# Performance work log

Measured on AMD Instinct MI355X. Metric: run time of the kernel, lower is better.

The kernel has to match this reference:

```python
import jax, jax.numpy as jnp
import numpy as np

H = 128            # hidden_channels
HM = 2 * H         # _inner_mlp_mult * H
N = 50000          # num nodes
E = 400000         # num edges
M = 800000         # num node-edge incidences (2 per edge)
BN_EPS = 1e-5


def _bn_relu(x, g, b):
    # BatchNorm1d in training mode: population stats over the batch dim, then affine + ReLU
    m = x.mean(0)
    v = ((x - m) ** 2).mean(0)
    return jax.nn.relu((x - m) * jax.lax.rsqrt(v + BN_EPS) * g + b)


def setup_inputs() -> dict:
    key = jax.random.key(0)
    ks = jax.random.split(key, 12)
    node_rep = jax.random.normal(ks[0], (N, H), dtype=jnp.float32)
    edge_rep = jax.random.normal(ks[1], (E, H), dtype=jnp.float32)
    src = jax.random.randint(ks[2], (M,), 0, N, dtype=jnp.int32)
    dst = jax.random.randint(ks[3], (M,), 0, E, dtype=jnp.int32)
    node2edge_index = jnp.stack([src, dst], 0)

    def lin(k, fan_in, fan_out):
        return jax.random.normal(k, (fan_in, fan_out), dtype=jnp.float32) / np.sqrt(fan_in)

    return {
        "node_rep": node_rep,
        "edge_rep": edge_rep,
        "node2edge_index": node2edge_index,
        # lvl_mlp_1: Linear(2H->H, no bias), BN(H), ReLU
        "Wa": lin(ks[4], 2 * H, H), "ga": jnp.ones((H,)), "ba": jnp.zeros((H,)),
        # lvl_mlp_2: Linear(H->2H), BN, ReLU, Linear(2H->H), BN, ReLU
        "Wb1": lin(ks[5], H, HM), "gb1": jnp.ones((HM,)), "bb1": jnp.zeros((HM,)),
        "Wb2": lin(ks[6], HM, H), "gb2": jnp.ones((H,)), "bb2": jnp.zeros((H,)),
        # lift_mlp: Linear(H->2H), BN, ReLU, Linear(2H->H), BN, ReLU
        "Wl1": lin(ks[7], H, HM), "gl1": jnp.ones((HM,)), "bl1": jnp.zeros((HM,)),
        "Wl2": lin(ks[8], HM, H), "gl2": jnp.ones((H,)), "bl2": jnp.zeros((H,)),
        "eps1": jnp.zeros(()), "eps2": jnp.zeros(()),
    }


def reference(node_rep, edge_rep, node2edge_index,
              Wa, ga, ba,
              Wb1, gb1, bb1, Wb2, gb2, bb2,
              Wl1, gl1, bl1, Wl2, gl2, bl2,
              eps1, eps2):
    src = node2edge_index[0]  # node index per incidence
    dst = node2edge_index[1]  # edge index per incidence

    # node -> edge gather + scatter_sum
    node2edge_val = node_rep[src]                                   # [M, H]
    lift_aggr = jax.ops.segment_sum(node2edge_val, dst, num_segments=E)  # [E, H]

    # lvl_mlp_1 on concatenated edge features
    lvl_aggr_edge = _bn_relu(jnp.concatenate([lift_aggr, edge_rep], -1) @ Wa, ga, ba)  # [E, H]

    # edge -> node gather + scatter_sum
    lvl_aggr = jax.ops.segment_sum(lvl_aggr_edge[dst], src, num_segments=N)  # [N, H]

    # lvl_mlp_2
    hn = (1.0 + eps1) * node_rep + lvl_aggr
    node_out = _bn_relu(_bn_relu(hn @ Wb1, gb1, bb1) @ Wb2, gb2, bb2)

    # lift_mlp
    he = (1.0 + eps2) * edge_rep + lift_aggr
    edge_out = _bn_relu(_bn_relu(he @ Wl1, gl1, bl1) @ Wl2, gl2, bl2)

    return node_out, edge_out
```

## Files before the change

### kernel.cpp

```cpp
#include <hip/hip_runtime.h>
#include <cstdint>
#include <cstddef>


typedef __bf16 bf16_t;
typedef __bf16 bf16x2 __attribute__((ext_vector_type(2)));
typedef __bf16 bf16x4 __attribute__((ext_vector_type(4)));
typedef __bf16 bf16x8 __attribute__((ext_vector_type(8)));
typedef float f32x4 __attribute__((ext_vector_type(4)));

__device__ __forceinline__ void atomAddF(float* p, float v) {
  unsafeAtomicAdd(p, v);
}


__global__ __launch_bounds__(256) void k_hist(
    const int* __restrict__ src, const int* __restrict__ dst, int M,
    int* __restrict__ cnt_e, int* __restrict__ cnt_n) {
  int i = blockIdx.x * blockDim.x + threadIdx.x;
  if (i >= M) return;
  atomicAdd(cnt_e + dst[i], 1);
  atomicAdd(cnt_n + src[i], 1);
}

__global__ __launch_bounds__(256) void k_scan_block(
    const int* __restrict__ in, int* __restrict__ out, int* __restrict__ bsum,
    int L) {
  __shared__ int sh[256];
  int t = threadIdx.x;
  int base = (blockIdx.x * 256 + t) * 4;
  int v[4];
#pragma unroll
  for (int j = 0; j < 4; ++j) v[j] = (base + j < L) ? in[base + j] : 0;
  int tsum = v[0] + v[1] + v[2] + v[3];
  sh[t] = tsum;
  __syncthreads();
#pragma unroll
  for (int off = 1; off < 256; off <<= 1) {
    int x = (t >= off) ? sh[t - off] : 0;
    __syncthreads();
    sh[t] += x;
    __syncthreads();
  }
  int excl = sh[t] - tsum;
  if (t == 255) bsum[blockIdx.x] = sh[255];
  int run = excl;
#pragma unroll
  for (int j = 0; j < 4; ++j) {
    if (base + j < L) out[base + j] = run;
    run += v[j];
  }
}

__global__ __launch_bounds__(1024) void k_scan_top(int* __restrict__ bsum,
                                                   int nb) {
  __shared__ int sh[1024];
  __shared__ int running;
  int t = threadIdx.x;
  if (t == 0) running = 0;
  __syncthreads();
  for (int c = 0; c < nb; c += 1024) {
    int i = c + t;
    int v = (i < nb) ? bsum[i] : 0;
    sh[t] = v;
    __syncthreads();
#pragma unroll
    for (int off = 1; off < 1024; off <<= 1) {
      int x = (t >= off) ? sh[t - off] : 0;
      __syncthreads();
      sh[t] += x;
      __syncthreads();
    }
    int r = running;
    if (i < nb) bsum[i] = r + sh[t] - v;
    __syncthreads();
    if (t == 1023) running = r + sh[1023];
    __syncthreads();
  }
}

__global__ __launch_bounds__(256) void k_scan_add(int* __restrict__ out,
                                                  const int* __restrict__ bsum,
                                                  int L) {
  int base = (blockIdx.x * 256 + threadIdx.x) * 4;
  int add = bsum[blockIdx.x];
#pragma unroll
  for (int j = 0; j < 4; ++j)
    if (base + j < L) out[base + j] += add;
}

__global__ void k_settail(int* off_e, int E, int* off_n, int N, int M) {
  off_e[E] = M;
  off_n[N] = M;
}

__global__ __launch_bounds__(256) void k_fill(
    const int* __restrict__ src, const int* __restrict__ dst, int M,
    const int* __restrict__ off_e, int* __restrict__ fill_e,
    int* __restrict__ csr_e, const int* __restrict__ off_n,
    int* __restrict__ fill_n, int* __restrict__ csr_n) {
  int i = blockIdx.x * blockDim.x + threadIdx.x;
  if (i >= M) return;
  int s = src[i], d = dst[i];
  int pe = off_e[d] + atomicAdd(fill_e + d, 1);
  csr_e[pe] = s;
  int pn = off_n[s] + atomicAdd(fill_n + s, 1);
  csr_n[pn] = d;
}

__global__ __launch_bounds__(256) void k_wconv(const float* __restrict__ W,
                                               bf16_t* __restrict__ Wt, int K,
                                               int NC) {
  int idx = blockIdx.x * blockDim.x + threadIdx.x;
  if (idx >= K * NC) return;
  int k = idx / NC, n = idx % NC;
  Wt[(size_t)n * K + k] = (bf16_t)W[idx];
}

__global__ __launch_bounds__(256) void k_gather1(
    const float* __restrict__ node, const int* __restrict__ off_e,
    const int* __restrict__ csr_e, bf16_t* __restrict__ lift, int E) {
  int e = blockIdx.x * 8 + (threadIdx.x >> 5);
  if (e >= E) return;
  int l = threadIdx.x & 31;
  int b = off_e[e], en = off_e[e + 1];
  float4 acc = make_float4(0.f, 0.f, 0.f, 0.f);
  for (int j = b; j < en; ++j) {
    int r = csr_e[j];
    float4 v = *(const float4*)(node + (size_t)r * 128 + l * 4);
    acc.x += v.x; acc.y += v.y; acc.z += v.z; acc.w += v.w;
  }
  bf16x4 o;
  o[0] = (bf16_t)acc.x; o[1] = (bf16_t)acc.y;
  o[2] = (bf16_t)acc.z; o[3] = (bf16_t)acc.w;
  *(bf16x4*)(lift + (size_t)e * 128 + l * 4) = o;
}

__global__ __launch_bounds__(256) void k_gather2(
    const bf16_t* __restrict__ Y1, const float* __restrict__ st,
    const float* __restrict__ node, const int* __restrict__ off_n,
    const int* __restrict__ csr_n, const float* __restrict__ eps1p,
    bf16_t* __restrict__ hn, int N) {
  int n = blockIdx.x * 16 + (threadIdx.x >> 4);
  if (n >= N) return;
  int l = threadIdx.x & 15;
  float a1 = 1.0f + eps1p[0];
  float4 s0 = *(const float4*)(st + l * 8);
  float4 s1 = *(const float4*)(st + l * 8 + 4);
  float4 t0 = *(const float4*)(st + 128 + l * 8);
  float4 t1 = *(const float4*)(st + 128 + l * 8 + 4);
  float acc[8] = {0.f, 0.f, 0.f, 0.f, 0.f, 0.f, 0.f, 0.f};
  int b = off_n[n], en = off_n[n + 1];
  for (int j = b; j < en; ++j) {
    int r = csr_n[j];
    bf16x8 y = *(const bf16x8*)(Y1 + (size_t)r * 128 + l * 8);
    acc[0] += fmaxf(fmaf((float)y[0], s0.x, t0.x), 0.f);
    acc[1] += fmaxf(fmaf((float)y[1], s0.y, t0.y), 0.f);
    acc[2] += fmaxf(fmaf((float)y[2], s0.z, t0.z), 0.f);
    acc[3] += fmaxf(fmaf((float)y[3], s0.w, t0.w), 0.f);
    acc[4] += fmaxf(fmaf((float)y[4], s1.x, t1.x), 0.f);
    acc[5] += fmaxf(fmaf((float)y[5], s1.y, t1.y), 0.f);
    acc[6] += fmaxf(fmaf((float)y[6], s1.z, t1.z), 0.f);
    acc[7] += fmaxf(fmaf((float)y[7], s1.w, t1.w), 0.f);
  }
  float4 n0 = *(const float4*)(node + (size_t)n * 128 + l * 8);
  float4 n1 = *(const float4*)(node + (size_t)n * 128 + l * 8 + 4);
  bf16x8 hb;
  hb[0] = (bf16_t)fmaf(a1, n0.x, acc[0]);
  hb[1] = (bf16_t)fmaf(a1, n0.y, acc[1]);
  hb[2] = (bf16_t)fmaf(a1, n0.z, acc[2]);
  hb[3] = (bf16_t)fmaf(a1, n0.w, acc[3]);
  hb[4] = (bf16_t)fmaf(a1, n1.x, acc[4]);
  hb[5] = (bf16_t)fmaf(a1, n1.y, acc[5]);
  hb[6] = (bf16_t)fmaf(a1, n1.z, acc[6]);
  hb[7] = (bf16_t)fmaf(a1, n1.w, acc[7]);
  *(bf16x8*)(hn + (size_t)n * 128 + l * 8) = hb;
}


__global__ void k_bnfin(const float* __restrict__ sums, int C, int R,
                        const float* __restrict__ g, const float* __restrict__ b,
                        float* __restrict__ st) {
  int c = blockIdx.x * blockDim.x + threadIdx.x;
  if (c >= C) return;
  float invR = 1.f / (float)R;
  float mean = sums[c] * invR;
  float var = fmaxf(sums[C + c] * invR - mean * mean, 0.f);
  float s = g[c] * rsqrtf(var + 1e-5f);
  st[c] = s;
  st[C + c] = fmaf(-mean, s, b[c]);
}

__global__ __launch_bounds__(256) void k_bnrelu_out(
    const bf16_t* __restrict__ Y, const float* __restrict__ st, long R,
    float* __restrict__ out) {
  long t = (long)blockIdx.x * blockDim.x + threadIdx.x;
  long idx = t * 8;
  if (idx >= R * 128) return;
  int c = (int)(idx & 127);
  bf16x8 y = *(const bf16x8*)(Y + idx);
  float4 s0 = *(const float4*)(st + c);
  float4 s1 = *(const float4*)(st + c + 4);
  float4 t0 = *(const float4*)(st + 128 + c);
  float4 t1 = *(const float4*)(st + 128 + c + 4);
  float4 o0, o1;
  o0.x = fmaxf(fmaf((float)y[0], s0.x, t0.x), 0.f);
  o0.y = fmaxf(fmaf((float)y[1], s0.y, t0.y), 0.f);
  o0.z = fmaxf(fmaf((float)y[2], s0.z, t0.z), 0.f);
  o0.w = fmaxf(fmaf((float)y[3], s0.w, t0.w), 0.f);
  o1.x = fmaxf(fmaf((float)y[4], s1.x, t1.x), 0.f);
  o1.y = fmaxf(fmaf((float)y[5], s1.y, t1.y), 0.f);
  o1.z = fmaxf(fmaf((float)y[6], s1.z, t1.z), 0.f);
  o1.w = fmaxf(fmaf((float)y[7], s1.w, t1.w), 0.f);
  *(float4*)(out + idx) = o0;
  *(float4*)(out + idx + 4) = o1;
}

#define LDSTR 40

template <int TRANSFORM>
__global__ __launch_bounds__(256) void k_mfma_gemm(
    const bf16_t* __restrict__ A, const bf16_t* __restrict__ Wt,
    const float* __restrict__ st, float* __restrict__ gstats,
    bf16_t* __restrict__ Y, int R, int K, int NCtot) {
  __shared__ bf16_t As[128 * LDSTR];
  __shared__ bf16_t Bs[128 * LDSTR];
  const int tid = threadIdx.x;
  const int wave = tid >> 6;
  const int lane = tid & 63;
  const int quad = lane >> 4;
  const int l16 = lane & 15;
  const int wm = wave & 1;
  const int wn = wave >> 1;
  const int r0 = blockIdx.x * 128;
  const int n0 = blockIdx.y * 128;

  f32x4 acc[4][4] = {};
  const int srow = tid >> 2;
  const int sk = (tid & 3) * 8;

  for (int k0 = 0; k0 < K; k0 += 32) {
#pragma unroll
    for (int p = 0; p < 2; ++p) {
      int row = p * 64 + srow;
      int gr = r0 + row;
      if (gr >= R) gr = R - 1;
      bf16x8 v = *(const bf16x8*)(A + (size_t)gr * K + k0 + sk);
      if (TRANSFORM) {
        bf16x8 o;
#pragma unroll
        for (int i = 0; i < 8; ++i) {
          float f = (float)v[i];
          float s = st[k0 + sk + i];
          float b = st[K + k0 + sk + i];
          o[i] = (bf16_t)fmaxf(fmaf(f, s, b), 0.f);
        }
        v = o;
      }
      *(bf16x8*)&As[row * LDSTR + sk] = v;
    }
#pragma unroll
    for (int p = 0; p < 2; ++p) {
      int row = p * 64 + srow;
      bf16x8 v = *(const bf16x8*)(Wt + (size_t)(n0 + row) * K + k0 + sk);
      *(bf16x8*)&Bs[row * LDSTR + sk] = v;
    }
    __syncthreads();
    bf16x8 af[4], bfr[4];
#pragma unroll
    for (int i = 0; i < 4; ++i)
      af[i] = *(const bf16x8*)&As[(wm * 64 + i * 16 + l16) * LDSTR + quad * 8];
#pragma unroll
    for (int j = 0; j < 4; ++j)
      bfr[j] = *(const bf16x8*)&Bs[(wn * 64 + j * 16 + l16) * LDSTR + quad * 8];
#pragma unroll
    for (int i = 0; i < 4; ++i)
#pragma unroll
      for (int j = 0; j < 4; ++j)
        acc[i][j] = __builtin_amdgcn_mfma_f32_16x16x32_bf16(af[i], bfr[j],
                                                            acc[i][j], 0, 0, 0);
    __syncthreads();
  }

  float csum[4] = {0.f, 0.f, 0.f, 0.f};
  float csq[4] = {0.f, 0.f, 0.f, 0.f};
#pragma unroll
  for (int i = 0; i < 4; ++i) {
    int baseRow = r0 + wm * 64 + i * 16 + quad * 4;
#pragma unroll
    for (int reg = 0; reg < 4; ++reg) {
      int row = baseRow + reg;
      if (row < R) {
#pragma unroll
        for (int j = 0; j < 4; ++j) {
          float v = acc[i][j][reg];
          int col = n0 + wn * 64 + j * 16 + l16;
          Y[(size_t)row * NCtot + col] = (bf16_t)v;
          csum[j] += v;
          csq[j] += v * v;
        }
      }
    }
  }
  __syncthreads();
  float* Ssum = (float*)As;
  float* Ssq = (float*)As + 1024;
  int contrib = wm * 4 + quad;
#pragma unroll
  for (int j = 0; j < 4; ++j) {
    int c = wn * 64 + j * 16 + l16;
    Ssum[c * 8 + contrib] = csum[j];
    Ssq[c * 8 + contrib] = csq[j];
  }
  __syncthreads();
  if (tid < 128) {
    float s = 0.f;
#pragma unroll
    for (int k = 0; k < 8; ++k) s += Ssum[tid * 8 + k];
    atomAddF(gstats + n0 + tid, s);
  } else {
    int c = tid - 128;
    float q = 0.f;
#pragma unroll
    for (int k = 0; k < 8; ++k) q += Ssq[c * 8 + k];
    atomAddF(gstats + NCtot + n0 + c, q);
  }
}

__global__ __launch_bounds__(256) void k_mfma_gemm_cat(
    const bf16_t* __restrict__ lift, const float* __restrict__ edge,
    const bf16_t* __restrict__ Wt, const float* __restrict__ eps2p,
    float* __restrict__ gstats, bf16_t* __restrict__ Y,
    bf16_t* __restrict__ he, int R) {
  __shared__ bf16_t As[128 * LDSTR];
  __shared__ bf16_t Bs[128 * LDSTR];
  const int tid = threadIdx.x;
  const int wave = tid >> 6;
  const int lane = tid & 63;
  const int quad = lane >> 4;
  const int l16 = lane & 15;
  const int wm = wave & 1;
  const int wn = wave >> 1;
  const int r0 = blockIdx.x * 128;
  const float a2 = 1.0f + eps2p[0];

  f32x4 acc[4][4] = {};
  const int srow = tid >> 2;
  const int sk = (tid & 3) * 8;
  bf16x8 lreg[4][2];

  for (int ph = 0; ph < 8; ++ph) {
    const int k0 = ph * 32;
#pragma unroll
    for (int p = 0; p < 2; ++p) {
      int row = p * 64 + srow;
      int gr = r0 + row;
      if (gr >= R) gr = R - 1;
      bf16x8 v;
      if (ph < 4) {
        v = *(const bf16x8*)(lift + (size_t)gr * 128 + k0 + sk);
        lreg[ph][p] = v;
      } else {
        const int kk = k0 - 128;
        float4 e0 = *(const float4*)(edge + (size_t)gr * 128 + kk + sk);
        float4 e1 = *(const float4*)(edge + (size_t)gr * 128 + kk + sk + 4);
        const float ef[8] = {e0.x, e0.y, e0.z, e0.w, e1.x, e1.y, e1.z, e1.w};
        bf16x8 lv = lreg[ph - 4][p];
        bf16x8 hv;
#pragma unroll
        for (int i = 0; i < 8; ++i) {
          v[i] = (bf16_t)ef[i];
          hv[i] = (bf16_t)fmaf(a2, ef[i], (float)lv[i]);
        }
        *(bf16x8*)(he + (size_t)gr * 128 + kk + sk) = hv;
      }
      *(bf16x8*)&As[row * LDSTR + sk] = v;
    }
#pragma unroll
    for (int p = 0; p < 2; ++p) {
      int row = p * 64 + srow;
      bf16x8 v = *(const bf16x8*)(Wt + (size_t)row * 256 + k0 + sk);
      *(bf16x8*)&Bs[row * LDSTR + sk] = v;
    }
    __syncthreads();
    bf16x8 af[4], bfr[4];
#pragma unroll
    for (int i = 0; i < 4; ++i)
      af[i] = *(const bf16x8*)&As[(wm * 64 + i * 16 + l16) * LDSTR + quad * 8];
#pragma unroll
    for (int j = 0; j < 4; ++j)
      bfr[j] = *(const bf16x8*)&Bs[(wn * 64 + j * 16 + l16) * LDSTR + quad * 8];
#pragma unroll
    for (int i = 0; i < 4; ++i)
#pragma unroll
      for (int j = 0; j < 4; ++j)
        acc[i][j] = __builtin_amdgcn_mfma_f32_16x16x32_bf16(af[i], bfr[j],
                                                            acc[i][j], 0, 0, 0);
    __syncthreads();
  }

  float csum[4] = {0.f, 0.f, 0.f, 0.f};
  float csq[4] = {0.f, 0.f, 0.f, 0.f};
#pragma unroll
  for (int i = 0; i < 4; ++i) {
    int baseRow = r0 + wm * 64 + i * 16 + quad * 4;
#pragma unroll
    for (int reg = 0; reg < 4; ++reg) {
      int row = baseRow + reg;
      if (row < R) {
#pragma unroll
        for (int j = 0; j < 4; ++j) {
          float v = acc[i][j][reg];
          int col = wn * 64 + j * 16 + l16;
          Y[(size_t)row * 128 + col] = (bf16_t)v;
          csum[j] += v;
          csq[j] += v * v;
        }
      }
    }
  }
  __syncthreads();
  float* Ssum = (float*)As;
  float* Ssq = (float*)As + 1024;
  int contrib = wm * 4 + quad;
#pragma unroll
  for (int j = 0; j < 4; ++j) {
    int c = wn * 64 + j * 16 + l16;
    Ssum[c * 8 + contrib] = csum[j];
    Ssq[c * 8 + contrib] = csq[j];
  }
  __syncthreads();
  if (tid < 128) {
    float s = 0.f;
#pragma unroll
    for (int k = 0; k < 8; ++k) s += Ssum[tid * 8 + k];
    atomAddF(gstats + tid, s);
  } else {
    int c = tid - 128;
    float q = 0.f;
#pragma unroll
    for (int k = 0; k < 8; ++k) q += Ssq[c * 8 + k];
    atomAddF(gstats + 128 + c, q);
  }
}


extern "C" void kernel_launch(void* const* d_in, const int* in_sizes, int n_in,
                              void* d_out, int out_size, void* d_ws,
                              size_t ws_size, hipStream_t stream) {
  const float* node_rep = (const float*)d_in[0];
  const float* edge_rep = (const float*)d_in[1];
  const int* n2e = (const int*)d_in[2];
  const float* Wa = (const float*)d_in[3];
  const float* ga = (const float*)d_in[4];
  const float* ba = (const float*)d_in[5];
  const float* Wb1 = (const float*)d_in[6];
  const float* gb1 = (const float*)d_in[7];
  const float* bb1 = (const float*)d_in[8];
  const float* Wb2 = (const float*)d_in[9];
  const float* gb2 = (const float*)d_in[10];
  const float* bb2 = (const float*)d_in[11];
  const float* Wl1 = (const float*)d_in[12];
  const float* gl1 = (const float*)d_in[13];
  const float* bl1 = (const float*)d_in[14];
  const float* Wl2 = (const float*)d_in[15];
  const float* gl2 = (const float*)d_in[16];
  const float* bl2 = (const float*)d_in[17];
  const float* eps1 = (const float*)d_in[18];
  const float* eps2 = (const float*)d_in[19];

  const int N = in_sizes[0] / 128;
  const int E = in_sizes[1] / 128;
  const int M = in_sizes[2] / 2;
  const int* srcI = n2e;
  const int* dstI = n2e + M;

  char* wsb = (char*)d_ws;
  size_t off = 0;
  auto alloc = [&](size_t bytes) {
    void* p = wsb + off;
    off += (bytes + 255) & ~(size_t)255;
    return p;
  };
  bf16_t* lift = (bf16_t*)alloc((size_t)E * 128 * 2);
  bf16_t* he   = (bf16_t*)alloc((size_t)E * 128 * 2);
  bf16_t* Y1   = (bf16_t*)alloc((size_t)E * 128 * 2);
  bf16_t* Ze   = (bf16_t*)alloc((size_t)E * 256 * 2);
  bf16_t* Y2e  = (bf16_t*)alloc((size_t)E * 128 * 2);
  bf16_t* hn   = (bf16_t*)alloc((size_t)N * 128 * 2);
  bf16_t* Zn   = (bf16_t*)alloc((size_t)N * 256 * 2);
  bf16_t* Y2n  = (bf16_t*)alloc((size_t)N * 128 * 2);
  bf16_t* Wa_t  = (bf16_t*)alloc(256 * 128 * 2);
  bf16_t* Wb1_t = (bf16_t*)alloc(128 * 256 * 2);
  bf16_t* Wb2_t = (bf16_t*)alloc(256 * 128 * 2);
  bf16_t* Wl1_t = (bf16_t*)alloc(128 * 256 * 2);
  bf16_t* Wl2_t = (bf16_t*)alloc(256 * 128 * 2);
  int* zbase  = (int*)alloc(((size_t)E * 2 + (size_t)N * 2 + 8192) * 4);
  int* cnt_e  = zbase;
  int* fill_e = zbase + E;
  int* cnt_n  = zbase + 2 * (size_t)E;
  int* fill_n = zbase + 2 * (size_t)E + N;
  float* stats = (float*)(zbase + 2 * (size_t)E + 2 * (size_t)N);
  int* off_e  = (int*)alloc((size_t)(E + 1) * 4);
  int* csr_e  = (int*)alloc((size_t)M * 4);
  int* off_n  = (int*)alloc((size_t)(N + 1) * 4);
  int* csr_n  = (int*)alloc((size_t)M * 4);
  int* bsumE  = (int*)alloc(4096 * 4);
  int* bsumN  = (int*)alloc(4096 * 4);

  float* sum_a  = stats + 0;
  float* st_a   = stats + 256;
  float* sum_b1 = stats + 512;
  float* st_b1  = stats + 1024;
  float* sum_b2 = stats + 1536;
  float* st_b2  = stats + 1792;
  float* sum_l1 = stats + 2048;
  float* st_l1  = stats + 2560;
  float* sum_l2 = stats + 3072;
  float* st_l2  = stats + 3328;

  float* node_out = (float*)d_out;
  float* edge_out = (float*)d_out + (size_t)N * 128;

  hipMemsetAsync(zbase, 0, ((size_t)E * 2 + (size_t)N * 2 + 8192) * 4, stream);

  k_hist<<<(M + 255) / 256, 256, 0, stream>>>(srcI, dstI, M, cnt_e, cnt_n);
  const int nbE = (E + 1023) / 1024;
  const int nbN = (N + 1023) / 1024;
  k_scan_block<<<nbE, 256, 0, stream>>>(cnt_e, off_e, bsumE, E);
  k_scan_top<<<1, 1024, 0, stream>>>(bsumE, nbE);
  k_scan_add<<<nbE, 256, 0, stream>>>(off_e, bsumE, E);
  k_scan_block<<<nbN, 256, 0, stream>>>(cnt_n, off_n, bsumN, N);
  k_scan_top<<<1, 1024, 0, stream>>>(bsumN, nbN);
  k_scan_add<<<nbN, 256, 0, stream>>>(off_n, bsumN, N);
  k_settail<<<1, 1, 0, stream>>>(off_e, E, off_n, N, M);
  k_fill<<<(M + 255) / 256, 256, 0, stream>>>(srcI, dstI, M, off_e, fill_e,
                                              csr_e, off_n, fill_n, csr_n);

  k_wconv<<<128, 256, 0, stream>>>(Wa, Wa_t, 256, 128);
  k_wconv<<<128, 256, 0, stream>>>(Wb1, Wb1_t, 128, 256);
  k_wconv<<<128, 256, 0, stream>>>(Wb2, Wb2_t, 256, 128);
  k_wconv<<<128, 256, 0, stream>>>(Wl1, Wl1_t, 128, 256);
  k_wconv<<<128, 256, 0, stream>>>(Wl2, Wl2_t, 256, 128);

  k_gather1<<<(E + 7) / 8, 256, 0, stream>>>(node_rep, off_e, csr_e, lift, E);

  k_mfma_gemm_cat<<<dim3((E + 127) / 128), 256, 0, stream>>>(
      lift, edge_rep, Wa_t, eps2, sum_a, Y1, he, E);
  k_bnfin<<<1, 256, 0, stream>>>(sum_a, 128, E, ga, ba, st_a);

  k_gather2<<<(N + 15) / 16, 256, 0, stream>>>(Y1, st_a, node_rep, off_n,
                                               csr_n, eps1, hn, N);

  k_mfma_gemm<0><<<dim3((N + 127) / 128, 2), 256, 0, stream>>>(
      hn, Wb1_t, nullptr, sum_b1, Zn, N, 128, 256);
  k_bnfin<<<1, 256, 0, stream>>>(sum_b1, 256, N, gb1, bb1, st_b1);
  k_mfma_gemm<1><<<dim3((N + 127) / 128, 1), 256, 0, stream>>>(
      Zn, Wb2_t, st_b1, sum_b2, Y2n, N, 256, 128);
  k_bnfin<<<1, 256, 0, stream>>>(sum_b2, 128, N, gb2, bb2, st_b2);
  {
    long total = ((long)N * 128 + 7) / 8;
    k_bnrelu_out<<<(int)((total + 255) / 256), 256, 0, stream>>>(Y2n, st_b2, N,
                                                                 node_out);
  }

  k_mfma_gemm<0><<<dim3((E + 127) / 128, 2), 256, 0, stream>>>(
      he, Wl1_t, nullptr, sum_l1, Ze, E, 128, 256);
  k_bnfin<<<1, 256, 0, stream>>>(sum_l1, 256, E, gl1, bl1, st_l1);
  k_mfma_gemm<1><<<dim3((E + 127) / 128, 1), 256, 0, stream>>>(
      Ze, Wl2_t, st_l1, sum_l2, Y2e, E, 256, 128);
  k_bnfin<<<1, 256, 0, stream>>>(sum_l2, 128, E, gl2, bl2, st_l2);
  {
    long total = ((long)E * 128 + 7) / 8;
    k_bnrelu_out<<<(int)((total + 255) / 256), 256, 0, stream>>>(Y2e, st_l2, E,
                                                                 edge_out);
  }
}
```

Before: 1.201 ms.

## Keep whole weight matrix in LDS and stream 16-row tiles persistently

Replaces the 128x128 tiled MFMA GEMMs with persistent kernels that load the full transposed weight into XOR-swizzled LDS once per block. Each wave then processes 16-row A tiles straight from global memory into registers, prefetching the next tile, and computes every output column. BN statistics are reduced with wave shuffles instead of an LDS pass. This removes the per-K-step A staging through LDS and the barriers, and lets the two column tiles of the 128->256 GEMM share one A read, but it uses 64KB of LDS per block and caps the grid at 512 blocks, which limits occupancy.

```diff
diff --git a/kernel.cpp b/kernel.cpp
--- a/kernel.cpp
+++ b/kernel.cpp
@@ -216,202 +216,201 @@
   *(float4*)(out + idx + 4) = o1;
 }
 
-#define LDSTR 40
-
-template <int TRANSFORM>
-__global__ __launch_bounds__(256) void k_mfma_gemm(
+template <int K, int NC, int TRANSFORM>
+__global__ __launch_bounds__(256, 2) void k_gemm_nb(
     const bf16_t* __restrict__ A, const bf16_t* __restrict__ Wt,
     const float* __restrict__ st, float* __restrict__ gstats,
-    bf16_t* __restrict__ Y, int R, int K, int NCtot) {
-  __shared__ bf16_t As[128 * LDSTR];
-  __shared__ bf16_t Bs[128 * LDSTR];
+    bf16_t* __restrict__ Y, int R) {
+  constexpr int K2 = K * 2;
+  constexpr int KF = K / 32;
+  constexpr int CT = NC / 16;
+  __shared__ bf16_t Bs[NC * K];
   const int tid = threadIdx.x;
+  for (int p = tid * 16; p < NC * K2; p += 4096) {
+    const int col = p / K2;
+    const int kb = p & (K2 - 1);
+    bf16x8 v = *(const bf16x8*)((const char*)Wt + p);
+    *(bf16x8*)((char*)Bs + col * K2 + (kb ^ ((col & 7) << 4))) = v;
+  }
+  __syncthreads();
+
   const int wave = tid >> 6;
   const int lane = tid & 63;
   const int quad = lane >> 4;
   const int l16 = lane & 15;
-  const int wm = wave & 1;
-  const int wn = wave >> 1;
-  const int r0 = blockIdx.x * 128;
-  const int n0 = blockIdx.y * 128;
-
-  f32x4 acc[4][4] = {};
-  const int srow = tid >> 2;
-  const int sk = (tid & 3) * 8;
-
-  for (int k0 = 0; k0 < K; k0 += 32) {
-#pragma unroll
-    for (int p = 0; p < 2; ++p) {
-      int row = p * 64 + srow;
-      int gr = r0 + row;
-      if (gr >= R) gr = R - 1;
-      bf16x8 v = *(const bf16x8*)(A + (size_t)gr * K + k0 + sk);
-      if (TRANSFORM) {
-        bf16x8 o;
-#pragma unroll
-        for (int i = 0; i < 8; ++i) {
-          float f = (float)v[i];
-          float s = st[k0 + sk + i];
-          float b = st[K + k0 + sk + i];
-          o[i] = (bf16_t)fmaxf(fmaf(f, s, b), 0.f);
-        }
-        v = o;
+  const int ntiles = (R + 15) >> 4;
+  const int tstep = gridDim.x * 4;
+
+  float csum[CT], csq[CT];
+#pragma unroll
+  for (int j = 0; j < CT; ++j) { csum[j] = 0.f; csq[j] = 0.f; }
+
+  bf16x8 af[KF];
+  auto loadA = [&](int t) {
+    int row = t * 16 + l16;
+    if (row >= R) row = R - 1;
+    const bf16_t* ap = A + (size_t)row * K + quad * 8;
+#pragma unroll
+    for (int f = 0; f < KF; ++f) af[f] = *(const bf16x8*)(ap + f * 32);
+  };
+
+  const int t0 = blockIdx.x * 4 + wave;
+  loadA(t0);
+  for (int t = t0; t < ntiles; t += tstep) {
+    bf16x8 cf[KF];
+    if (TRANSFORM) {
+#pragma unroll
+      for (int f = 0; f < KF; ++f) {
+        const int kb = f * 32 + quad * 8;
+        const float4 s0 = *(const float4*)(st + kb);
+        const float4 s1 = *(const float4*)(st + kb + 4);
+        const float4 b0 = *(const float4*)(st + K + kb);
+        const float4 b1 = *(const float4*)(st + K + kb + 4);
+        bf16x8 v = af[f], o;
+        o[0] = (bf16_t)fmaxf(fmaf((float)v[0], s0.x, b0.x), 0.f);
+        o[1] = (bf16_t)fmaxf(fmaf((float)v[1], s0.y, b0.y), 0.f);
+        o[2] = (bf16_t)fmaxf(fmaf((float)v[2], s0.z, b0.z), 0.f);
+        o[3] = (bf16_t)fmaxf(fmaf((float)v[3], s0.w, b0.w), 0.f);
+        o[4] = (bf16_t)fmaxf(fmaf((float)v[4], s1.x, b1.x), 0.f);
+        o[5] = (bf16_t)fmaxf(fmaf((float)v[5], s1.y, b1.y), 0.f);
+        o[6] = (bf16_t)fmaxf(fmaf((float)v[6], s1.z, b1.z), 0.f);
+        o[7] = (bf16_t)fmaxf(fmaf((float)v[7], s1.w, b1.w), 0.f);
+        cf[f] = o;
       }
-      *(bf16x8*)&As[row * LDSTR + sk] = v;
-    }
-#pragma unroll
-    for (int p = 0; p < 2; ++p) {
-      int row = p * 64 + srow;
-      bf16x8 v = *(const bf16x8*)(Wt + (size_t)(n0 + row) * K + k0 + sk);
-      *(bf16x8*)&Bs[row * LDSTR + sk] = v;
-    }
-    __syncthreads();
-    bf16x8 af[4], bfr[4];
-#pragma unroll
-    for (int i = 0; i < 4; ++i)
-      af[i] = *(const bf16x8*)&As[(wm * 64 + i * 16 + l16) * LDSTR + quad * 8];
-#pragma unroll
-    for (int j = 0; j < 4; ++j)
-      bfr[j] = *(const bf16x8*)&Bs[(wn * 64 + j * 16 + l16) * LDSTR + quad * 8];
-#pragma unroll
-    for (int i = 0; i < 4; ++i)
-#pragma unroll
-      for (int j = 0; j < 4; ++j)
-        acc[i][j] = __builtin_amdgcn_mfma_f32_16x16x32_bf16(af[i], bfr[j],
-                                                            acc[i][j], 0, 0, 0);
-    __syncthreads();
-  }
-
-  float csum[4] = {0.f, 0.f, 0.f, 0.f};
-  float csq[4] = {0.f, 0.f, 0.f, 0.f};
-#pragma unroll
-  for (int i = 0; i < 4; ++i) {
-    int baseRow = r0 + wm * 64 + i * 16 + quad * 4;
-#pragma unroll
-    for (int reg = 0; reg < 4; ++reg) {
-      int row = baseRow + reg;
-      if (row < R) {
-#pragma unroll
-        for (int j = 0; j < 4; ++j) {
-          float v = acc[i][j][reg];
-          int col = n0 + wn * 64 + j * 16 + l16;
-          Y[(size_t)row * NCtot + col] = (bf16_t)v;
+    } else {
+#pragma unroll
+      for (int f = 0; f < KF; ++f) cf[f] = af[f];
+    }
+    loadA(t + tstep);
+
+    f32x4 acc[CT] = {};
+#pragma unroll
+    for (int j = 0; j < CT; ++j) {
+      const int colr = j * 16 + l16;
+      const char* bp = (const char*)Bs + colr * K2;
+      const int sw = (colr & 7) << 4;
+#pragma unroll
+      for (int f = 0; f < KF; ++f) {
+        bf16x8 bv = *(const bf16x8*)(bp + ((f * 64 + quad * 16) ^ sw));
+        acc[j] =
+            __builtin_amdgcn_mfma_f32_16x16x32_bf16(cf[f], bv, acc[j], 0, 0, 0);
+      }
+    }
+    const int r0 = t * 16 + quad * 4;
+#pragma unroll
+    for (int j = 0; j < CT; ++j) {
+      const int col = j * 16 + l16;
+#pragma unroll
+      for (int reg = 0; reg < 4; ++reg) {
+        const int row = r0 + reg;
+        if (row < R) {
+          const float v = acc[j][reg];
+          Y[(size_t)row * NC + col] = (bf16_t)v;
           csum[j] += v;
           csq[j] += v * v;
         }
       }
     }
   }
-  __syncthreads();
-  float* Ssum = (float*)As;
-  float* Ssq = (float*)As + 1024;
-  int contrib = wm * 4 + quad;
-#pragma unroll
-  for (int j = 0; j < 4; ++j) {
-    int c = wn * 64 + j * 16 + l16;
-    Ssum[c * 8 + contrib] = csum[j];
-    Ssq[c * 8 + contrib] = csq[j];
-  }
-  __syncthreads();
-  if (tid < 128) {
-    float s = 0.f;
-#pragma unroll
-    for (int k = 0; k < 8; ++k) s += Ssum[tid * 8 + k];
-    atomAddF(gstats + n0 + tid, s);
-  } else {
-    int c = tid - 128;
-    float q = 0.f;
-#pragma unroll
-    for (int k = 0; k < 8; ++k) q += Ssq[c * 8 + k];
-    atomAddF(gstats + NCtot + n0 + c, q);
-  }
-}
-
-__global__ __launch_bounds__(256) void k_mfma_gemm_cat(
+#pragma unroll
+  for (int j = 0; j < CT; ++j) {
+    float s = csum[j], q = csq[j];
+    s += __shfl_xor(s, 16, 64);
+    s += __shfl_xor(s, 32, 64);
+    q += __shfl_xor(q, 16, 64);
+    q += __shfl_xor(q, 32, 64);
+    if (quad == 0) {
+      atomAddF(gstats + j * 16 + l16, s);
+      atomAddF(gstats + NC + j * 16 + l16, q);
+    }
+  }
+}
+
+__global__ __launch_bounds__(256, 2) void k_gemm_cat_nb(
     const bf16_t* __restrict__ lift, const float* __restrict__ edge,
     const bf16_t* __restrict__ Wt, const float* __restrict__ eps2p,
     float* __restrict__ gstats, bf16_t* __restrict__ Y,
     bf16_t* __restrict__ he, int R) {
-  __shared__ bf16_t As[128 * LDSTR];
-  __shared__ bf16_t Bs[128 * LDSTR];
+  constexpr int K2 = 512;
+  __shared__ bf16_t Bs[128 * 256];
   const int tid = threadIdx.x;
+  for (int p = tid * 16; p < 128 * K2; p += 4096) {
+    const int col = p >> 9;
+    const int kb = p & 511;
+    bf16x8 v = *(const bf16x8*)((const char*)Wt + p);
+    *(bf16x8*)((char*)Bs + col * K2 + (kb ^ ((col & 7) << 4))) = v;
+  }
+  __syncthreads();
+
   const int wave = tid >> 6;
   const int lane = tid & 63;
   const int quad = lane >> 4;
   const int l16 = lane & 15;
-  const int wm = wave & 1;
-  const int wn = wave >> 1;
-  const int r0 = blockIdx.x * 128;
   const float a2 = 1.0f + eps2p[0];
-
-  f32x4 acc[4][4] = {};
-  const int srow = tid >> 2;
-  const int sk = (tid & 3) * 8;
-  bf16x8 lreg[4][2];
-
-  for (int ph = 0; ph < 8; ++ph) {
-    const int k0 = ph * 32;
-#pragma unroll
-    for (int p = 0; p < 2; ++p) {
-      int row = p * 64 + srow;
-      int gr = r0 + row;
-      if (gr >= R) gr = R - 1;
-      bf16x8 v;
-      if (ph < 4) {
-        v = *(const bf16x8*)(lift + (size_t)gr * 128 + k0 + sk);
-        lreg[ph][p] = v;
-      } else {
-        const int kk = k0 - 128;
-        float4 e0 = *(const float4*)(edge + (size_t)gr * 128 + kk + sk);
-        float4 e1 = *(const float4*)(edge + (size_t)gr * 128 + kk + sk + 4);
-        const float ef[8] = {e0.x, e0.y, e0.z, e0.w, e1.x, e1.y, e1.z, e1.w};
-        bf16x8 lv = lreg[ph - 4][p];
-        bf16x8 hv;
-#pragma unroll
-        for (int i = 0; i < 8; ++i) {
-          v[i] = (bf16_t)ef[i];
-          hv[i] = (bf16_t)fmaf(a2, ef[i], (float)lv[i]);
-        }
-        *(bf16x8*)(he + (size_t)gr * 128 + kk + sk) = hv;
+  const int ntiles = (R + 15) >> 4;
+  const int tstep = gridDim.x * 4;
+
+  float csum[8] = {}, csq[8] = {};
+  bf16x8 lf[4];
+  float4 ef0[4], ef1[4];
+  auto loadA = [&](int t) {
+    int row = t * 16 + l16;
+    if (row >= R) row = R - 1;
+    const bf16_t* lp = lift + (size_t)row * 128 + quad * 8;
+    const float* ep = edge + (size_t)row * 128 + quad * 8;
+#pragma unroll
+    for (int f = 0; f < 4; ++f) {
+      lf[f] = *(const bf16x8*)(lp + f * 32);
+      ef0[f] = *(const float4*)(ep + f * 32);
+      ef1[f] = *(const float4*)(ep + f * 32 + 4);
+    }
+  };
+
+  const int t0 = blockIdx.x * 4 + wave;
+  loadA(t0);
+  for (int t = t0; t < ntiles; t += tstep) {
+    const int rowc = t * 16 + l16;
+    const bool rok = rowc < R;
+    bf16x8 cf[8];
+#pragma unroll
+    for (int f = 0; f < 4; ++f) cf[f] = lf[f];
+#pragma unroll
+    for (int f = 0; f < 4; ++f) {
+      const float e[8] = {ef0[f].x, ef0[f].y, ef0[f].z, ef0[f].w,
+                          ef1[f].x, ef1[f].y, ef1[f].z, ef1[f].w};
+      bf16x8 v, hv;
+#pragma unroll
+      for (int i = 0; i < 8; ++i) {
+        v[i] = (bf16_t)e[i];
+        hv[i] = (bf16_t)fmaf(a2, e[i], (float)cf[f][i]);
       }
-      *(bf16x8*)&As[row * LDSTR + sk] = v;
-    }
-#pragma unroll
-    for (int p = 0; p < 2; ++p) {
-      int row = p * 64 + srow;
-      bf16x8 v = *(const bf16x8*)(Wt + (size_t)row * 256 + k0 + sk);
-      *(bf16x8*)&Bs[row * LDSTR + sk] = v;
-    }
-    __syncthreads();
-    bf16x8 af[4], bfr[4];
-#pragma unroll
-    for (int i = 0; i < 4; ++i)
-      af[i] = *(const bf16x8*)&As[(wm * 64 + i * 16 + l16) * LDSTR + quad * 8];
-#pragma unroll
-    for (int j = 0; j < 4; ++j)
-      bfr[j] = *(const bf16x8*)&Bs[(wn * 64 + j * 16 + l16) * LDSTR + quad * 8];
-#pragma unroll
-    for (int i = 0; i < 4; ++i)
-#pragma unroll
-      for (int j = 0; j < 4; ++j)
-        acc[i][j] = __builtin_amdgcn_mfma_f32_16x16x32_bf16(af[i], bfr[j],
-                                                            acc[i][j], 0, 0, 0);
-    __syncthreads();
-  }
-
-  float csum[4] = {0.f, 0.f, 0.f, 0.f};
-  float csq[4] = {0.f, 0.f, 0.f, 0.f};
-#pragma unroll
-  for (int i = 0; i < 4; ++i) {
-    int baseRow = r0 + wm * 64 + i * 16 + quad * 4;
-#pragma unroll
-    for (int reg = 0; reg < 4; ++reg) {
-      int row = baseRow + reg;
-      if (row < R) {
-#pragma unroll
-        for (int j = 0; j < 4; ++j) {
-          float v = acc[i][j][reg];
-          int col = wn * 64 + j * 16 + l16;
+      cf[4 + f] = v;
+      if (rok) *(bf16x8*)(he + (size_t)rowc * 128 + f * 32 + quad * 8) = hv;
+    }
+    loadA(t + tstep);
+
+    f32x4 acc[8] = {};
+#pragma unroll
+    for (int j = 0; j < 8; ++j) {
+      const int colr = j * 16 + l16;
+      const char* bp = (const char*)Bs + colr * K2;
+      const int sw = (colr & 7) << 4;
+#pragma unroll
+      for (int f = 0; f < 8; ++f) {
+        bf16x8 bv = *(const bf16x8*)(bp + ((f * 64 + quad * 16) ^ sw));
+        acc[j] =
+            __builtin_amdgcn_mfma_f32_16x16x32_bf16(cf[f], bv, acc[j], 0, 0, 0);
+      }
+    }
+    const int r0 = t * 16 + quad * 4;
+#pragma unroll
+    for (int j = 0; j < 8; ++j) {
+      const int col = j * 16 + l16;
+#pragma unroll
+      for (int reg = 0; reg < 4; ++reg) {
+        const int row = r0 + reg;
+        if (row < R) {
+          const float v = acc[j][reg];
           Y[(size_t)row * 128 + col] = (bf16_t)v;
           csum[j] += v;
           csq[j] += v * v;
@@ -419,28 +418,17 @@
       }
     }
   }
-  __syncthreads();
-  float* Ssum = (float*)As;
-  float* Ssq = (float*)As + 1024;
-  int contrib = wm * 4 + quad;
-#pragma unroll
-  for (int j = 0; j < 4; ++j) {
-    int c = wn * 64 + j * 16 + l16;
-    Ssum[c * 8 + contrib] = csum[j];
-    Ssq[c * 8 + contrib] = csq[j];
-  }
-  __syncthreads();
-  if (tid < 128) {
-    float s = 0.f;
-#pragma unroll
-    for (int k = 0; k < 8; ++k) s += Ssum[tid * 8 + k];
-    atomAddF(gstats + tid, s);
-  } else {
-    int c = tid - 128;
-    float q = 0.f;
-#pragma unroll
-    for (int k = 0; k < 8; ++k) q += Ssq[c * 8 + k];
-    atomAddF(gstats + 128 + c, q);
+#pragma unroll
+  for (int j = 0; j < 8; ++j) {
+    float s = csum[j], q = csq[j];
+    s += __shfl_xor(s, 16, 64);
+    s += __shfl_xor(s, 32, 64);
+    q += __shfl_xor(q, 16, 64);
+    q += __shfl_xor(q, 32, 64);
+    if (quad == 0) {
+      atomAddF(gstats + j * 16 + l16, s);
+      atomAddF(gstats + 128 + j * 16 + l16, q);
+    }
   }
 }
 
@@ -543,20 +531,25 @@
   k_wconv<<<128, 256, 0, stream>>>(Wl1, Wl1_t, 128, 256);
   k_wconv<<<128, 256, 0, stream>>>(Wl2, Wl2_t, 256, 128);
 
+  int ntE = (E + 15) / 16, gE = (ntE + 3) / 4;
+  if (gE > 512) gE = 512;
+  int ntN = (N + 15) / 16, gN = (ntN + 3) / 4;
+  if (gN > 512) gN = 512;
+
   k_gather1<<<(E + 7) / 8, 256, 0, stream>>>(node_rep, off_e, csr_e, lift, E);
 
-  k_mfma_gemm_cat<<<dim3((E + 127) / 128), 256, 0, stream>>>(
-      lift, edge_rep, Wa_t, eps2, sum_a, Y1, he, E);
+  k_gemm_cat_nb<<<gE, 256, 0, stream>>>(lift, edge_rep, Wa_t, eps2, sum_a, Y1,
+                                        he, E);
   k_bnfin<<<1, 256, 0, stream>>>(sum_a, 128, E, ga, ba, st_a);
 
   k_gather2<<<(N + 15) / 16, 256, 0, stream>>>(Y1, st_a, node_rep, off_n,
                                                csr_n, eps1, hn, N);
 
-  k_mfma_gemm<0><<<dim3((N + 127) / 128, 2), 256, 0, stream>>>(
-      hn, Wb1_t, nullptr, sum_b1, Zn, N, 128, 256);
+  k_gemm_nb<128, 256, 0><<<gN, 256, 0, stream>>>(hn, Wb1_t, nullptr, sum_b1,
+                                                 Zn, N);
   k_bnfin<<<1, 256, 0, stream>>>(sum_b1, 256, N, gb1, bb1, st_b1);
-  k_mfma_gemm<1><<<dim3((N + 127) / 128, 1), 256, 0, stream>>>(
-      Zn, Wb2_t, st_b1, sum_b2, Y2n, N, 256, 128);
+  k_gemm_nb<256, 128, 1><<<gN, 256, 0, stream>>>(Zn, Wb2_t, st_b1, sum_b2,
+                                                 Y2n, N);
   k_bnfin<<<1, 256, 0, stream>>>(sum_b2, 128, N, gb2, bb2, st_b2);
   {
     long total = ((long)N * 128 + 7) / 8;
@@ -564,11 +557,11 @@
                                                                  node_out);
   }
 
-  k_mfma_gemm<0><<<dim3((E + 127) / 128, 2), 256, 0, stream>>>(
-      he, Wl1_t, nullptr, sum_l1, Ze, E, 128, 256);
+  k_gemm_nb<128, 256, 0><<<gE, 256, 0, stream>>>(he, Wl1_t, nullptr, sum_l1,
+                                                 Ze, E);
   k_bnfin<<<1, 256, 0, stream>>>(sum_l1, 256, E, gl1, bl1, st_l1);
-  k_mfma_gemm<1><<<dim3((E + 127) / 128, 1), 256, 0, stream>>>(
-      Ze, Wl2_t, st_l1, sum_l2, Y2e, E, 256, 128);
+  k_gemm_nb<256, 128, 1><<<gE, 256, 0, stream>>>(Ze, Wl2_t, st_l1, sum_l2,
+                                                 Y2e, E);
   k_bnfin<<<1, 256, 0, stream>>>(sum_l2, 128, E, gl2, bl2, st_l2);
   {
     long total = ((long)E * 128 + 7) / 8;
```

Result: slower. 1.716 ms (+42.8%).
